# Performance work log

Hardware: AMD Instinct MI355X
Metric: run time of the kernel (lower is better)

## Reference

```python
import jax, jax.numpy as jnp
import numpy as np

N = 100000   # nodes
E = 1600000  # edges
F = 128      # feature dim == Dense units
R = 50       # relations
BN_EPS = 1e-3  # keras BatchNormalization default epsilon


def setup_inputs() -> dict:
    key = jax.random.key(0)
    ks = jax.random.split(key, 8)
    x = jax.random.normal(ks[0], (N, F), dtype=jnp.float32)
    edge_rows = jax.random.randint(ks[1], (E,), 0, N, dtype=jnp.int32)
    edge_cols = jax.random.randint(ks[2], (E,), 0, N, dtype=jnp.int32)
    edge_vals = jax.random.uniform(ks[3], (E,), dtype=jnp.float32)
    rel_ids = jax.random.randint(ks[4], (E,), 0, R, dtype=jnp.int32)
    relation_coeffs = jax.random.uniform(ks[5], (R,), dtype=jnp.float32)
    coeff_kernel = jax.random.normal(ks[6], (N, 1), dtype=jnp.float32) * 0.05
    dense_kernel = jax.random.normal(ks[7], (F, F), dtype=jnp.float32) / np.sqrt(F).astype(np.float32)
    dense_bias = jnp.zeros((F,), dtype=jnp.float32)
    bn_gamma = jnp.ones((F,), dtype=jnp.float32)
    bn_beta = jnp.zeros((F,), dtype=jnp.float32)
    bn_mean = jnp.zeros((F,), dtype=jnp.float32)
    bn_var = jnp.ones((F,), dtype=jnp.float32)
    return {
        "x": x, "edge_rows": edge_rows, "edge_cols": edge_cols,
        "edge_vals": edge_vals, "rel_ids": rel_ids,
        "relation_coeffs": relation_coeffs, "coeff_kernel": coeff_kernel,
        "dense_kernel": dense_kernel, "dense_bias": dense_bias,
        "bn_gamma": bn_gamma, "bn_beta": bn_beta,
        "bn_mean": bn_mean, "bn_var": bn_var,
    }


def reference(x, edge_rows, edge_cols, edge_vals, rel_ids,
              relation_coeffs, coeff_kernel, dense_kernel, dense_bias,
              bn_gamma, bn_beta, bn_mean, bn_var):
    # BatchNorm (inference: moving statistics)
    h = (x - bn_mean) * jax.lax.rsqrt(bn_var + BN_EPS) * bn_gamma + bn_beta  # [N, F]
    # relation_coeff_adj2: edge weight = A.values * (rel_coeffs[rel] + 1)^-1
    w = edge_vals / (relation_coeffs[rel_ids] + 1.0)  # [E]
    # SpMM: out[i] = sum_{(i,j) in edges} w_e * h[j]
    msgs = w[:, None] * h[edge_cols]                   # [E, F]
    agg = jax.ops.segment_sum(msgs, edge_rows, num_segments=N)  # [N, F]
    # CoeffLayer(mul=True): inputs * (kernel + 1)
    pre = agg + h * (coeff_kernel + 1.0)               # [N, F]
    # Dense
    return pre @ dense_kernel + dense_bias             # [N, F]
```

## Files before the change

kernel.cpp:

```cpp
#include <hip/hip_runtime.h>
#include <stdint.h>

#define N_NODES 100000
#define N_EDGES 1600000
#define FDIM 128
#define NREL 50
#define BN_EPS 1e-3f
#define N_PAD 100096
#define NBUCK 782
#define EPB 8192
#define NBLK 196
#define HBLK 6250
#define LEDCAP 2816
#define SCAP 3712
#define NSG 1563

typedef short short8_t __attribute__((ext_vector_type(8)));
typedef float f32x4_t __attribute__((ext_vector_type(4)));

__device__ __forceinline__ uint32_t f2bf(float f) {
    union { float f; uint32_t u; } v; v.f = f;
    uint32_t u = v.u;
    return (u + 0x7FFFu + ((u >> 16) & 1u)) >> 16;
}
__device__ __forceinline__ float bflo(uint32_t p) {
    union { uint32_t u; float f; } v; v.u = p << 16; return v.f;
}
__device__ __forceinline__ float bfhi(uint32_t p) {
    union { uint32_t u; float f; } v; v.u = p & 0xFFFF0000u; return v.f;
}

__global__ __launch_bounds__(512) void pre_kernel(
        const float* __restrict__ x, const int* __restrict__ rows,
        const int* __restrict__ cols, const float* __restrict__ vals,
        const int* __restrict__ rels, const float* __restrict__ relc,
        const float* __restrict__ gamma, const float* __restrict__ beta,
        const float* __restrict__ mean, const float* __restrict__ var,
        const float* __restrict__ W,
        uint2* __restrict__ h, uint16_t* __restrict__ WT,
        int* __restrict__ gcur, uint2* __restrict__ staging) {
    __shared__ int lh[NBUCK];
    __shared__ float lrel[NREL];
    int b = blockIdx.x, t = threadIdx.x;
    if (b < NBLK) {
        if (t < NREL) lrel[t] = 1.0f / (relc[t] + 1.0f);
        for (int i = t; i < NBUCK; i += 512) lh[i] = 0;
        __syncthreads();
        int e0 = b * EPB, e1 = min(e0 + EPB, N_EDGES);
        for (int e = e0 + t; e < e1; e += 512)
            atomicAdd(&lh[rows[e] >> 7], 1);
        __syncthreads();
        for (int i = t; i < NBUCK; i += 512) {
            int c = lh[i];
            int base = c ? atomicAdd(&gcur[i], c) : 0;
            lh[i] = i * SCAP + base;
        }
        __syncthreads();
        for (int e = e0 + t; e < e1; e += 512) {
            int r = rows[e];
            float w = vals[e] * lrel[rels[e]];
            int p = atomicAdd(&lh[r >> 7], 1);
            uint2 s;
            s.x = (uint32_t)cols[e] | ((uint32_t)(r & 127) << 20);
            s.y = __float_as_uint(w);
            staging[p] = s;
        }
    } else if (b == NBLK) {
        for (int idx = t; idx < FDIM * FDIM; idx += 512) {
            int f = idx >> 7, k = idx & 127;
            WT[idx] = (uint16_t)f2bf(W[k * FDIM + f]);
        }
    } else {
        int i4 = (b - NBLK - 1) * 512 + t;
        int cg = (i4 & 31) * 4;
        float4 xv = ((const float4*)x)[i4];
        float4 g4 = *(const float4*)(gamma + cg);
        float4 b4 = *(const float4*)(beta + cg);
        float4 m4 = *(const float4*)(mean + cg);
        float4 v4 = *(const float4*)(var + cg);
        float s0 = g4.x * rsqrtf(v4.x + BN_EPS);
        float s1 = g4.y * rsqrtf(v4.y + BN_EPS);
        float s2 = g4.z * rsqrtf(v4.z + BN_EPS);
        float s3 = g4.w * rsqrtf(v4.w + BN_EPS);
        uint2 o;
        o.x = f2bf((xv.x - m4.x) * s0 + b4.x) | (f2bf((xv.y - m4.y) * s1 + b4.y) << 16);
        o.y = f2bf((xv.z - m4.z) * s2 + b4.z) | (f2bf((xv.w - m4.w) * s3 + b4.w) << 16);
        h[i4] = o;
    }
}

__global__ __launch_bounds__(256) void bucket_kernel(
        const int* __restrict__ gcur, uint2* __restrict__ staging,
        uint2* __restrict__ rowrange) {
    __shared__ uint2 led[LEDCAP];
    __shared__ int lh[128];
    __shared__ int sm[128];
    __shared__ int lcur[128];
    int b = blockIdx.x, r0 = b << 7, t = threadIdx.x;
    int nrows = min(128, N_NODES - r0);
    int cnt = min(gcur[b], LEDCAP);
    uint2* sg = staging + (size_t)b * SCAP;
    if (t < 128) lh[t] = 0;
    __syncthreads();
    for (int e = t; e < cnt; e += 256) {
        uint2 s = sg[e];
        led[e] = s;
        atomicAdd(&lh[(s.x >> 20) & 127], 1);
    }
    __syncthreads();
    int v = (t < 128) ? lh[t] : 0;
    int pv = (v + 7) & ~7;
    if (t < 128) sm[t] = pv;
    __syncthreads();
    for (int off = 1; off < 128; off <<= 1) {
        int xv = 0;
        if (t < 128 && t >= off) xv = sm[t - off];
        __syncthreads();
        if (t < 128) sm[t] += xv;
        __syncthreads();
    }
    int sbase = b * SCAP;
    int start = 0;
    if (t < 128) {
        start = sbase + sm[t] - pv;
        lcur[t] = start;
        if (t < nrows) {
            uint2 rr; rr.x = (uint32_t)start; rr.y = (uint32_t)(start + pv);
            rowrange[r0 + t] = rr;
        }
    }
    __syncthreads();
    for (int e = t; e < cnt; e += 256) {
        uint2 s = led[e];
        int rl = (s.x >> 20) & 127;
        int p = atomicAdd(&lcur[rl], 1);
        uint2 o; o.x = s.x & 0xFFFFF; o.y = s.y;
        staging[p] = o;
    }
    if (t < 128) {
        uint2 z; z.x = 0; z.y = 0;
        for (int k = v; k < pv; ++k) staging[start + k] = z;
    }
}

__global__ __launch_bounds__(256, 6) void sg_kernel(
        const uint32_t* __restrict__ h, const uint2* __restrict__ rowrange,
        const uint2* __restrict__ scolw, const float* __restrict__ ck,
        const uint16_t* __restrict__ WT, const float* __restrict__ bias,
        float* __restrict__ out) {
    __shared__ uint32_t lp[64 * 64];
    int wv = threadIdx.x >> 6;
    int lane = threadIdx.x & 63;
    int row0 = blockIdx.x * 64;

    for (int ri = 0; ri < 16; ++ri) {
        int rl = wv * 16 + ri;
        int row = row0 + rl;
        float ax = 0.f, ay = 0.f;
        if (row < N_NODES) {
            uint2 rg = rowrange[row];
            int e  = __builtin_amdgcn_readfirstlane((int)rg.x);
            int e1 = __builtin_amdgcn_readfirstlane((int)rg.y);
            uint32_t p = h[(uint32_t)row * 64u + lane];
            float coef = ck[row] + 1.0f;
            ax = coef * bflo(p);
            ay = coef * bfhi(p);
            for (; e < e1; e += 8) {
                const uint4* ep = (const uint4*)(scolw + e);
                uint4 eA = ep[0], eB = ep[1], eC = ep[2], eD = ep[3];
                uint32_t q0 = h[eA.x * 64u + lane];
                uint32_t q1 = h[eA.z * 64u + lane];
                uint32_t q2 = h[eB.x * 64u + lane];
                uint32_t q3 = h[eB.z * 64u + lane];
                uint32_t q4 = h[eC.x * 64u + lane];
                uint32_t q5 = h[eC.z * 64u + lane];
                uint32_t q6 = h[eD.x * 64u + lane];
                uint32_t q7 = h[eD.z * 64u + lane];
                float w0 = __uint_as_float(eA.y), w1 = __uint_as_float(eA.w);
                float w2 = __uint_as_float(eB.y), w3 = __uint_as_float(eB.w);
                float w4 = __uint_as_float(eC.y), w5 = __uint_as_float(eC.w);
                float w6 = __uint_as_float(eD.y), w7 = __uint_as_float(eD.w);
                ax += w0 * bflo(q0); ay += w0 * bfhi(q0);
                ax += w1 * bflo(q1); ay += w1 * bfhi(q1);
                ax += w2 * bflo(q2); ay += w2 * bfhi(q2);
                ax += w3 * bflo(q3); ay += w3 * bfhi(q3);
                ax += w4 * bflo(q4); ay += w4 * bfhi(q4);
                ax += w5 * bflo(q5); ay += w5 * bfhi(q5);
                ax += w6 * bflo(q6); ay += w6 * bfhi(q6);
                ax += w7 * bflo(q7); ay += w7 * bfhi(q7);
            }
        }
        uint32_t pk = f2bf(ax) | (f2bf(ay) << 16);
        lp[rl * 64 + (lane ^ ((rl & 7) << 2))] = pk;
    }
    __syncthreads();

    int m = lane & 15, q = lane >> 4;
    int rowm = wv * 16 + m;
    short8_t a[4];
#pragma unroll
    for (int t = 0; t < 4; ++t) {
        int w0 = (q * 4 + t * 16) ^ ((rowm & 7) << 2);
        a[t] = *(const short8_t*)&lp[rowm * 64 + w0];
    }
    int row0m = row0 + wv * 16;
    for (int ct = 0; ct < 8; ++ct) {
        int col0 = ct * 16;
        const uint16_t* brow = WT + (size_t)(col0 + m) * FDIM + q * 8;
        f32x4_t acc = {0.f, 0.f, 0.f, 0.f};
#pragma unroll
        for (int t = 0; t < 4; ++t) {
            short8_t bb = *(const short8_t*)(brow + t * 32);
            acc = __builtin_amdgcn_mfma_f32_16x16x32_bf16(a[t], bb, acc, 0, 0, 0);
        }
        float bs = bias[col0 + m];
#pragma unroll
        for (int r = 0; r < 4; ++r) {
            int row = row0m + q * 4 + r;
            if (row < N_NODES)
                out[(size_t)row * FDIM + col0 + m] = acc[r] + bs;
        }
    }
}

extern "C" void kernel_launch(void* const* d_in, const int* in_sizes, int n_in,
                              void* d_out, int out_size, void* d_ws, size_t ws_size,
                              hipStream_t stream) {
    const float* x     = (const float*)d_in[0];
    const int*   erows = (const int*)d_in[1];
    const int*   ecols = (const int*)d_in[2];
    const float* evals = (const float*)d_in[3];
    const int*   erels = (const int*)d_in[4];
    const float* relc  = (const float*)d_in[5];
    const float* ck    = (const float*)d_in[6];
    const float* W     = (const float*)d_in[7];
    const float* bias  = (const float*)d_in[8];
    const float* gamma = (const float*)d_in[9];
    const float* beta  = (const float*)d_in[10];
    const float* mean  = (const float*)d_in[11];
    const float* var   = (const float*)d_in[12];
    float* out = (float*)d_out;

    char* wp = (char*)d_ws;
    auto alloc = [&](size_t bytes) {
        char* p = wp;
        wp += (bytes + 255) & ~(size_t)255;
        return (void*)p;
    };
    uint16_t* h      = (uint16_t*)alloc((size_t)N_PAD * FDIM * 2);
    uint2* staging   = (uint2*)alloc((size_t)NBUCK * SCAP * 8);
    uint2* rowrange  = (uint2*)alloc((size_t)N_PAD * 8);
    int* gcur        = (int*)alloc((size_t)NBUCK * 4);
    uint16_t* WT     = (uint16_t*)alloc(FDIM * FDIM * 2);
    if ((size_t)(wp - (char*)d_ws) > ws_size) return;

    hipMemsetAsync(gcur, 0, (size_t)NBUCK * 4, stream);
    pre_kernel<<<NBLK + 1 + HBLK, 512, 0, stream>>>(
        x, erows, ecols, evals, erels, relc, gamma, beta, mean, var, W,
        (uint2*)h, WT, gcur, staging);
    bucket_kernel<<<NBUCK, 256, 0, stream>>>(gcur, staging, rowrange);
    sg_kernel<<<NSG, 256, 0, stream>>>((const uint32_t*)h, rowrange, staging, ck,
                                       WT, bias, out);
}
```

Baseline: 270.7 us.

## Restructure gather-SpMM into 16-row blocks with two interleaved rows per wave

The gather kernel now launches 6250 blocks of 512 threads, each handling 16 rows. Each wave processes two rows at once with interleaved edge loops, padded to 4 edges instead of 8, and then computes one 16-column MFMA tile of the dense projection. The aim is more memory-level parallelism, better load balance and less padding waste in the irregular gathers. In exchange the W tile reuse per block drops, the staging capacity per bucket shrinks, and the N_NODES bounds checks are removed, which relies on the padded buffers.

```diff
diff --git a/kernel.cpp b/kernel.cpp
--- a/kernel.cpp
+++ b/kernel.cpp
@@ -12,8 +12,9 @@
 #define NBLK 196
 #define HBLK 6250
 #define LEDCAP 2816
-#define SCAP 3712
-#define NSG 1563
+#define SLACK 384
+#define SCAP 3200
+#define NSG 6250
 
 typedef short short8_t __attribute__((ext_vector_type(8)));
 typedef float f32x4_t __attribute__((ext_vector_type(4)));
@@ -109,7 +110,7 @@
     }
     __syncthreads();
     int v = (t < 128) ? lh[t] : 0;
-    int pv = (v + 7) & ~7;
+    int pv = (v + 3) & ~3;
     if (t < 128) sm[t] = pv;
     __syncthreads();
     for (int off = 1; off < 128; off <<= 1) {
@@ -143,84 +144,110 @@
     }
 }
 
-__global__ __launch_bounds__(256, 6) void sg_kernel(
+__global__ __launch_bounds__(512, 8) void sg_kernel(
         const uint32_t* __restrict__ h, const uint2* __restrict__ rowrange,
         const uint2* __restrict__ scolw, const float* __restrict__ ck,
         const uint16_t* __restrict__ WT, const float* __restrict__ bias,
         float* __restrict__ out) {
-    __shared__ uint32_t lp[64 * 64];
+    __shared__ uint32_t lp[16 * 64];
     int wv = threadIdx.x >> 6;
     int lane = threadIdx.x & 63;
-    int row0 = blockIdx.x * 64;
-
-    for (int ri = 0; ri < 16; ++ri) {
-        int rl = wv * 16 + ri;
-        int row = row0 + rl;
-        float ax = 0.f, ay = 0.f;
-        if (row < N_NODES) {
-            uint2 rg = rowrange[row];
-            int e  = __builtin_amdgcn_readfirstlane((int)rg.x);
-            int e1 = __builtin_amdgcn_readfirstlane((int)rg.y);
-            uint32_t p = h[(uint32_t)row * 64u + lane];
-            float coef = ck[row] + 1.0f;
-            ax = coef * bflo(p);
-            ay = coef * bfhi(p);
-            for (; e < e1; e += 8) {
-                const uint4* ep = (const uint4*)(scolw + e);
-                uint4 eA = ep[0], eB = ep[1], eC = ep[2], eD = ep[3];
-                uint32_t q0 = h[eA.x * 64u + lane];
-                uint32_t q1 = h[eA.z * 64u + lane];
-                uint32_t q2 = h[eB.x * 64u + lane];
-                uint32_t q3 = h[eB.z * 64u + lane];
-                uint32_t q4 = h[eC.x * 64u + lane];
-                uint32_t q5 = h[eC.z * 64u + lane];
-                uint32_t q6 = h[eD.x * 64u + lane];
-                uint32_t q7 = h[eD.z * 64u + lane];
-                float w0 = __uint_as_float(eA.y), w1 = __uint_as_float(eA.w);
-                float w2 = __uint_as_float(eB.y), w3 = __uint_as_float(eB.w);
-                float w4 = __uint_as_float(eC.y), w5 = __uint_as_float(eC.w);
-                float w6 = __uint_as_float(eD.y), w7 = __uint_as_float(eD.w);
-                ax += w0 * bflo(q0); ay += w0 * bfhi(q0);
-                ax += w1 * bflo(q1); ay += w1 * bfhi(q1);
-                ax += w2 * bflo(q2); ay += w2 * bfhi(q2);
-                ax += w3 * bflo(q3); ay += w3 * bfhi(q3);
-                ax += w4 * bflo(q4); ay += w4 * bfhi(q4);
-                ax += w5 * bflo(q5); ay += w5 * bfhi(q5);
-                ax += w6 * bflo(q6); ay += w6 * bfhi(q6);
-                ax += w7 * bflo(q7); ay += w7 * bfhi(q7);
-            }
-        }
-        uint32_t pk = f2bf(ax) | (f2bf(ay) << 16);
-        lp[rl * 64 + (lane ^ ((rl & 7) << 2))] = pk;
-    }
+    int row0 = blockIdx.x * 16;
+    int rA = row0 + wv * 2, rB = rA + 1;
+
+    uint2 ra = rowrange[rA];
+    uint2 rb = rowrange[rB];
+    int eA  = __builtin_amdgcn_readfirstlane((int)ra.x);
+    int e1A = __builtin_amdgcn_readfirstlane((int)ra.y);
+    int eB  = __builtin_amdgcn_readfirstlane((int)rb.x);
+    int e1B = __builtin_amdgcn_readfirstlane((int)rb.y);
+    uint32_t pA = h[(uint32_t)rA * 64u + lane];
+    uint32_t pB = h[(uint32_t)rB * 64u + lane];
+    float cA = ck[rA] + 1.0f, cB = ck[rB] + 1.0f;
+    float axA = cA * bflo(pA), ayA = cA * bfhi(pA);
+    float axB = cB * bflo(pB), ayB = cB * bfhi(pB);
+
+    while (eA < e1A && eB < e1B) {
+        const uint4* pa = (const uint4*)(scolw + eA);
+        const uint4* pb = (const uint4*)(scolw + eB);
+        uint4 a0 = pa[0], a1 = pa[1];
+        uint4 b0 = pb[0], b1 = pb[1];
+        uint32_t qa0 = h[a0.x * 64u + lane];
+        uint32_t qa1 = h[a0.z * 64u + lane];
+        uint32_t qa2 = h[a1.x * 64u + lane];
+        uint32_t qa3 = h[a1.z * 64u + lane];
+        uint32_t qb0 = h[b0.x * 64u + lane];
+        uint32_t qb1 = h[b0.z * 64u + lane];
+        uint32_t qb2 = h[b1.x * 64u + lane];
+        uint32_t qb3 = h[b1.z * 64u + lane];
+        float wa0 = __uint_as_float(a0.y), wa1 = __uint_as_float(a0.w);
+        float wa2 = __uint_as_float(a1.y), wa3 = __uint_as_float(a1.w);
+        float wb0 = __uint_as_float(b0.y), wb1 = __uint_as_float(b0.w);
+        float wb2 = __uint_as_float(b1.y), wb3 = __uint_as_float(b1.w);
+        axA += wa0 * bflo(qa0); ayA += wa0 * bfhi(qa0);
+        axA += wa1 * bflo(qa1); ayA += wa1 * bfhi(qa1);
+        axA += wa2 * bflo(qa2); ayA += wa2 * bfhi(qa2);
+        axA += wa3 * bflo(qa3); ayA += wa3 * bfhi(qa3);
+        axB += wb0 * bflo(qb0); ayB += wb0 * bfhi(qb0);
+        axB += wb1 * bflo(qb1); ayB += wb1 * bfhi(qb1);
+        axB += wb2 * bflo(qb2); ayB += wb2 * bfhi(qb2);
+        axB += wb3 * bflo(qb3); ayB += wb3 * bfhi(qb3);
+        eA += 4; eB += 4;
+    }
+    while (eA < e1A) {
+        const uint4* pa = (const uint4*)(scolw + eA);
+        uint4 a0 = pa[0], a1 = pa[1];
+        uint32_t qa0 = h[a0.x * 64u + lane];
+        uint32_t qa1 = h[a0.z * 64u + lane];
+        uint32_t qa2 = h[a1.x * 64u + lane];
+        uint32_t qa3 = h[a1.z * 64u + lane];
+        float wa0 = __uint_as_float(a0.y), wa1 = __uint_as_float(a0.w);
+        float wa2 = __uint_as_float(a1.y), wa3 = __uint_as_float(a1.w);
+        axA += wa0 * bflo(qa0); ayA += wa0 * bfhi(qa0);
+        axA += wa1 * bflo(qa1); ayA += wa1 * bfhi(qa1);
+        axA += wa2 * bflo(qa2); ayA += wa2 * bfhi(qa2);
+        axA += wa3 * bflo(qa3); ayA += wa3 * bfhi(qa3);
+        eA += 4;
+    }
+    while (eB < e1B) {
+        const uint4* pb = (const uint4*)(scolw + eB);
+        uint4 b0 = pb[0], b1 = pb[1];
+        uint32_t qb0 = h[b0.x * 64u + lane];
+        uint32_t qb1 = h[b0.z * 64u + lane];
+        uint32_t qb2 = h[b1.x * 64u + lane];
+        uint32_t qb3 = h[b1.z * 64u + lane];
+        float wb0 = __uint_as_float(b0.y), wb1 = __uint_as_float(b0.w);
+        float wb2 = __uint_as_float(b1.y), wb3 = __uint_as_float(b1.w);
+        axB += wb0 * bflo(qb0); ayB += wb0 * bfhi(qb0);
+        axB += wb1 * bflo(qb1); ayB += wb1 * bfhi(qb1);
+        axB += wb2 * bflo(qb2); ayB += wb2 * bfhi(qb2);
+        axB += wb3 * bflo(qb3); ayB += wb3 * bfhi(qb3);
+        eB += 4;
+    }
+    int rlA = wv * 2, rlB = rlA + 1;
+    lp[rlA * 64 + (lane ^ ((rlA & 7) << 2))] = f2bf(axA) | (f2bf(ayA) << 16);
+    lp[rlB * 64 + (lane ^ ((rlB & 7) << 2))] = f2bf(axB) | (f2bf(ayB) << 16);
     __syncthreads();
 
     int m = lane & 15, q = lane >> 4;
-    int rowm = wv * 16 + m;
     short8_t a[4];
 #pragma unroll
     for (int t = 0; t < 4; ++t) {
-        int w0 = (q * 4 + t * 16) ^ ((rowm & 7) << 2);
-        a[t] = *(const short8_t*)&lp[rowm * 64 + w0];
-    }
-    int row0m = row0 + wv * 16;
-    for (int ct = 0; ct < 8; ++ct) {
-        int col0 = ct * 16;
-        const uint16_t* brow = WT + (size_t)(col0 + m) * FDIM + q * 8;
-        f32x4_t acc = {0.f, 0.f, 0.f, 0.f};
+        int w0 = (q * 4 + t * 16) ^ ((m & 7) << 2);
+        a[t] = *(const short8_t*)&lp[m * 64 + w0];
+    }
+    int col0 = wv * 16;
+    const uint16_t* brow = WT + (size_t)(col0 + m) * FDIM + q * 8;
+    f32x4_t acc = {0.f, 0.f, 0.f, 0.f};
 #pragma unroll
-        for (int t = 0; t < 4; ++t) {
-            short8_t bb = *(const short8_t*)(brow + t * 32);
-            acc = __builtin_amdgcn_mfma_f32_16x16x32_bf16(a[t], bb, acc, 0, 0, 0);
-        }
-        float bs = bias[col0 + m];
+    for (int t = 0; t < 4; ++t) {
+        short8_t bb = *(const short8_t*)(brow + t * 32);
+        acc = __builtin_amdgcn_mfma_f32_16x16x32_bf16(a[t], bb, acc, 0, 0, 0);
+    }
+    float bs = bias[col0 + m];
 #pragma unroll
-        for (int r = 0; r < 4; ++r) {
-            int row = row0m + q * 4 + r;
-            if (row < N_NODES)
-                out[(size_t)row * FDIM + col0 + m] = acc[r] + bs;
-        }
-    }
+    for (int r = 0; r < 4; ++r)
+        out[(size_t)(row0 + q * 4 + r) * FDIM + col0 + m] = acc[r] + bs;
 }
 
 extern "C" void kernel_launch(void* const* d_in, const int* in_sizes, int n_in,
@@ -259,6 +286,6 @@
         x, erows, ecols, evals, erels, relc, gamma, beta, mean, var, W,
         (uint2*)h, WT, gcur, staging);
     bucket_kernel<<<NBUCK, 256, 0, stream>>>(gcur, staging, rowrange);
-    sg_kernel<<<NSG, 256, 0, stream>>>((const uint32_t*)h, rowrange, staging, ck,
+    sg_kernel<<<NSG, 512, 0, stream>>>((const uint32_t*)h, rowrange, staging, ck,
                                        WT, bias, out);
 }
```

Result: faster. 259.9 us (-4.0%).
